# Kernel tuning notes

Hardware: AMD Instinct MI355X
Metric: run time of the kernel (lower is better)

The kernel has to match this reference:

```python
import jax, jax.numpy as jnp
import numpy as np

NUM_SEQ, NUM_RES = 512, 768
MSA_C, PAIR_C, NUM_HEAD = 64, 128, 8
VALUE_DIM = MSA_C // NUM_HEAD
EPS = 1e-5


def _layernorm(x, scale, bias):
    mu = jnp.mean(x, axis=-1, keepdims=True)
    var = jnp.var(x, axis=-1, keepdims=True)
    return (x - mu) * jax.lax.rsqrt(var + EPS) * scale + bias


def setup_inputs() -> dict:
    key = jax.random.key(0)
    ks = jax.random.split(key, 8)
    act = jax.random.normal(ks[0], (NUM_SEQ, NUM_RES, MSA_C), dtype=jnp.float32)
    mask = jnp.ones((NUM_SEQ, NUM_RES), dtype=jnp.float32)
    pair_act = jax.random.normal(ks[1], (NUM_RES, NUM_RES, PAIR_C), dtype=jnp.float32)
    # learned params
    act_scale = jnp.ones((MSA_C,), jnp.float32)
    act_bias = jnp.zeros((MSA_C,), jnp.float32)
    pair_scale = jnp.ones((PAIR_C,), jnp.float32)
    pair_bias = jnp.zeros((PAIR_C,), jnp.float32)
    w_pair_logits = jax.random.normal(ks[2], (NUM_HEAD, PAIR_C), jnp.float32) * (PAIR_C ** -0.5)
    v_proj = jax.random.normal(ks[3], (MSA_C, NUM_HEAD, VALUE_DIM), jnp.float32) * (MSA_C ** -0.5)
    w_gate = jax.random.normal(ks[4], (MSA_C, MSA_C), jnp.float32) * (MSA_C ** -0.5)
    w_out = jax.random.normal(ks[5], (MSA_C, MSA_C), jnp.float32) * (MSA_C ** -0.5)
    return {
        "act": act, "mask": mask, "pair_act": pair_act,
        "act_scale": act_scale, "act_bias": act_bias,
        "pair_scale": pair_scale, "pair_bias": pair_bias,
        "w_pair_logits": w_pair_logits, "v_proj": v_proj,
        "w_gate": w_gate, "w_out": w_out,
    }


def reference(act, mask, pair_act, act_scale, act_bias, pair_scale, pair_bias,
              w_pair_logits, v_proj, w_gate, w_out):
    act = _layernorm(act, act_scale, act_bias)            # [b, k, i]
    pair = _layernorm(pair_act, pair_scale, pair_bias)    # [q, k, c]
    logits = jnp.einsum('qkc,hc->hqk', pair, w_pair_logits)  # [h, q, k]
    # mask reduced over MSA rows; torch casts to bf16 before the bias add
    mask_max = jnp.max(mask, axis=0).astype(jnp.bfloat16)    # [k]
    logits = logits + 1e9 * (mask_max.astype(logits.dtype) - 1.0)
    weights = jax.nn.softmax(logits, axis=-1)                # [h, q, k]
    v = jnp.einsum('bki,ihc->bkhc', act, v_proj)             # [b, k, h, c]
    v_avg = jnp.einsum('hqk,bkhc->bqhc', weights, v)         # [b, q, h, c]
    v_avg = v_avg.reshape(v_avg.shape[0], v_avg.shape[1], -1)  # [b, q, h*c]
    gate = jax.nn.sigmoid(act @ w_gate.T)
    return (v_avg * gate) @ w_out.T
```

## Files before the change

kernel.cpp:

```cpp
#include <hip/hip_runtime.h>
#include <hip/hip_bf16.h>

#define NSEQ 512
#define NRES 768
#define MSAC 64
#define PAIRC 128
#define NHEAD 8

typedef __attribute__((ext_vector_type(8))) short short8_t;
typedef __attribute__((ext_vector_type(4))) float f32x4;

__device__ __forceinline__ float bf2f(unsigned short u){
  return __uint_as_float(((unsigned int)u) << 16);
}
__device__ __forceinline__ unsigned short f2bf(float f){
  unsigned int x = __float_as_uint(f);
  x += 0x7fffu + ((x >> 16) & 1u);
  return (unsigned short)(x >> 16);
}
__device__ __forceinline__ void glds16(const void* g, void* l){
  __builtin_amdgcn_global_load_lds(
      (const __attribute__((address_space(1))) unsigned int*)g,
      (__attribute__((address_space(3))) unsigned int*)l, 16, 0, 0);
}

__global__ __launch_bounds__(256) void k_prep2(
    const float* __restrict__ mask, const float* __restrict__ vproj,
    const float* __restrict__ wgate, const float* __restrict__ wout,
    float* __restrict__ bias, unsigned short* __restrict__ WvT,
    unsigned short* __restrict__ WgT, unsigned short* __restrict__ WoH,
    unsigned short* __restrict__ WoL)
{
  const int bid = blockIdx.x, tid = threadIdx.x;
  if (bid < 12){
    __shared__ float red[4][64];
    const int kk = bid*64 + (tid & 63);
    const int bs = tid >> 6;
    float m = -1e30f;
    for (int b = bs; b < NSEQ; b += 4) m = fmaxf(m, mask[(size_t)b*NRES + kk]);
    red[bs][tid & 63] = m;
    __syncthreads();
    if (tid < 64){
      float mm = fmaxf(fmaxf(red[0][tid], red[1][tid]),
                       fmaxf(red[2][tid], red[3][tid]));
      bias[bid*64 + tid] = 1e9f * (bf2f(f2bf(mm)) - 1.0f);
    }
  } else {
    const int t = (bid - 12)*256 + tid;
    const int j = t >> 6, i = t & 63;
    WvT[t] = f2bf(vproj[i*64 + j]);
    WgT[t] = f2bf(wgate[t]);
    float wv = wout[t];
    unsigned short hh = f2bf(wv);
    WoH[t] = hh;
    WoL[t] = f2bf(wv - bf2f(hh));
  }
}

__global__ __launch_bounds__(256) void k_pairact(
    const float* __restrict__ pair, const float* __restrict__ pscale,
    const float* __restrict__ pbias, const float* __restrict__ wl,
    const float* __restrict__ mbias, unsigned short* __restrict__ weights,
    const float* __restrict__ act, const float* __restrict__ ascale,
    const float* __restrict__ abias, const unsigned short* __restrict__ WvT,
    const unsigned short* __restrict__ WgT, unsigned short* __restrict__ v,
    unsigned short* __restrict__ gate)
{
  __shared__ __align__(16) unsigned char sm[24576];
  const int bid = blockIdx.x;
  const int tid = threadIdx.x;

  if (bid < 768){
    float (*lg)[NRES] = (float (*)[NRES])sm;
    const int q = bid;
    const int wv = tid >> 6, lane = tid & 63;
    const int g = lane & 7;
    const int c0 = g * 16;

    float scl[16], bsl[16];
    #pragma unroll
    for (int i = 0; i < 4; ++i){
      float4 s4 = *(const float4*)(pscale + c0 + i*4);
      float4 b4 = *(const float4*)(pbias  + c0 + i*4);
      scl[4*i+0]=s4.x; scl[4*i+1]=s4.y; scl[4*i+2]=s4.z; scl[4*i+3]=s4.w;
      bsl[4*i+0]=b4.x; bsl[4*i+1]=b4.y; bsl[4*i+2]=b4.z; bsl[4*i+3]=b4.w;
    }
    unsigned int wp[8][8];
    #pragma unroll
    for (int h = 0; h < 8; ++h){
      #pragma unroll
      for (int jj = 0; jj < 8; ++jj){
        float2 w2 = *(const float2*)(wl + h*PAIRC + c0 + jj*2);
        wp[h][jj] = (unsigned int)f2bf(w2.x) | ((unsigned int)f2bf(w2.y) << 16);
      }
    }

    for (int it = 0; it < 24; ++it){
      int k = it*32 + wv*8 + (lane >> 3);
      const float* prow = pair + ((size_t)q * NRES + k) * PAIRC + c0;
      float x[16];
      #pragma unroll
      for (int i = 0; i < 4; ++i){
        float4 v4 = *(const float4*)(prow + i*4);
        x[4*i+0]=v4.x; x[4*i+1]=v4.y; x[4*i+2]=v4.z; x[4*i+3]=v4.w;
      }
      float s = 0.f, ss = 0.f;
      #pragma unroll
      for (int i = 0; i < 16; ++i){ s += x[i]; ss += x[i]*x[i]; }
      #pragma unroll
      for (int m = 1; m < 8; m <<= 1){
        s  += __shfl_xor(s,  m, 64);
        ss += __shfl_xor(ss, m, 64);
      }
      float mu  = s * (1.f/128.f);
      float var = ss * (1.f/128.f) - mu*mu;
      float rs  = rsqrtf(var + 1e-5f);
      #pragma unroll
      for (int i = 0; i < 16; ++i) x[i] = (x[i] - mu) * rs * scl[i] + bsl[i];
      float ph[8];
      #pragma unroll
      for (int h = 0; h < 8; ++h){
        float p = 0.f;
        #pragma unroll
        for (int jj = 0; jj < 8; ++jj){
          unsigned int w = wp[h][jj];
          float wlo = __uint_as_float(w << 16);
          float whi = __uint_as_float(w & 0xffff0000u);
          p += x[2*jj] * wlo + x[2*jj+1] * whi;
        }
        ph[h] = p;
      }
      #pragma unroll
      for (int h = 0; h < 8; ++h){
        #pragma unroll
        for (int m = 1; m < 8; m <<= 1) ph[h] += __shfl_xor(ph[h], m, 64);
      }
      #pragma unroll
      for (int h = 0; h < 8; ++h) if (g == h) lg[h][k] = ph[h];
    }
    __syncthreads();
    #pragma unroll
    for (int hh = 0; hh < 2; ++hh){
      int h = wv + hh*4;
      float mx = -1e30f;
      for (int kk = lane; kk < NRES; kk += 64) mx = fmaxf(mx, lg[h][kk] + mbias[kk]);
      #pragma unroll
      for (int m = 1; m < 64; m <<= 1) mx = fmaxf(mx, __shfl_xor(mx, m, 64));
      float sum = 0.f;
      for (int kk = lane; kk < NRES; kk += 64){
        float e = __expf(lg[h][kk] + mbias[kk] - mx);
        lg[h][kk] = e; sum += e;
      }
      #pragma unroll
      for (int m = 1; m < 64; m <<= 1) sum += __shfl_xor(sum, m, 64);
      float inv = 1.0f / sum;
      unsigned short* wrow = weights + ((size_t)h * NRES + q) * NRES;
      for (int kk = lane; kk < NRES; kk += 64) wrow[kk] = f2bf(lg[h][kk] * inv);
    }
  } else {
    unsigned short (*vt)[72] = (unsigned short (*)[72])sm;
    unsigned short (*gt)[72] = (unsigned short (*)[72])(sm + 9216);
    const int abid = bid - 768;
    const int b  = abid / 12;
    const int k0 = (abid % 12) * 64;
    const int w = tid >> 6, lane = tid & 63;
    const int lr = lane & 15;
    const int lc = lane >> 4;
    const int row = k0 + w*16 + lr;

    const float* arow = act + ((size_t)b*NRES + row)*MSAC;
    float x[2][8];
    #pragma unroll
    for (int s = 0; s < 2; ++s){
      float4 t0 = *(const float4*)(arow + s*32 + lc*8);
      float4 t1 = *(const float4*)(arow + s*32 + lc*8 + 4);
      x[s][0]=t0.x; x[s][1]=t0.y; x[s][2]=t0.z; x[s][3]=t0.w;
      x[s][4]=t1.x; x[s][5]=t1.y; x[s][6]=t1.z; x[s][7]=t1.w;
    }
    float ps = 0.f, pss = 0.f;
    #pragma unroll
    for (int s = 0; s < 2; ++s)
      #pragma unroll
      for (int e = 0; e < 8; ++e){ ps += x[s][e]; pss += x[s][e]*x[s][e]; }
    ps  += __shfl_xor(ps, 16, 64);  pss += __shfl_xor(pss, 16, 64);
    ps  += __shfl_xor(ps, 32, 64);  pss += __shfl_xor(pss, 32, 64);
    const float mu  = ps * (1.f/64.f);
    const float var = pss * (1.f/64.f) - mu*mu;
    const float rs  = rsqrtf(var + 1e-5f);

    short8_t a[2];
    #pragma unroll
    for (int s = 0; s < 2; ++s){
      float4 s0 = *(const float4*)(ascale + s*32 + lc*8);
      float4 s1 = *(const float4*)(ascale + s*32 + lc*8 + 4);
      float4 b0 = *(const float4*)(abias  + s*32 + lc*8);
      float4 b1 = *(const float4*)(abias  + s*32 + lc*8 + 4);
      const float sc[8] = {s0.x,s0.y,s0.z,s0.w,s1.x,s1.y,s1.z,s1.w};
      const float bs[8] = {b0.x,b0.y,b0.z,b0.w,b1.x,b1.y,b1.z,b1.w};
      #pragma unroll
      for (int e = 0; e < 8; ++e)
        a[s][e] = (short)f2bf((x[s][e] - mu)*rs*sc[e] + bs[e]);
    }

    short8_t bv[4][2], bg[4][2];
    #pragma unroll
    for (int mf = 0; mf < 4; ++mf){
      #pragma unroll
      for (int s = 0; s < 2; ++s){
        bv[mf][s] = *(const short8_t*)(WvT + (mf*16 + lr)*64 + s*32 + lc*8);
        bg[mf][s] = *(const short8_t*)(WgT + (mf*16 + lr)*64 + s*32 + lc*8);
      }
    }

    f32x4 accv[4], accg[4];
    #pragma unroll
    for (int mf = 0; mf < 4; ++mf){ accv[mf] = 0.f; accg[mf] = 0.f; }
    #pragma unroll
    for (int mf = 0; mf < 4; ++mf){
      #pragma unroll
      for (int s = 0; s < 2; ++s){
        accv[mf] = __builtin_amdgcn_mfma_f32_16x16x32_bf16(a[s], bv[mf][s], accv[mf], 0, 0, 0);
        accg[mf] = __builtin_amdgcn_mfma_f32_16x16x32_bf16(bg[mf][s], a[s], accg[mf], 0, 0, 0);
      }
    }

    #pragma unroll
    for (int mf = 0; mf < 4; ++mf){
      ushort4 ov;
      ov.x = f2bf(accv[mf][0]); ov.y = f2bf(accv[mf][1]);
      ov.z = f2bf(accv[mf][2]); ov.w = f2bf(accv[mf][3]);
      *(ushort4*)&vt[mf*16 + lr][w*16 + lc*4] = ov;
      ushort4 og;
      og.x = f2bf(1.0f/(1.0f + __expf(-accg[mf][0])));
      og.y = f2bf(1.0f/(1.0f + __expf(-accg[mf][1])));
      og.z = f2bf(1.0f/(1.0f + __expf(-accg[mf][2])));
      og.w = f2bf(1.0f/(1.0f + __expf(-accg[mf][3])));
      *(ushort4*)&gt[w*16 + lr][mf*16 + lc*4] = og;
    }
    __syncthreads();
    #pragma unroll
    for (int it = 0; it < 2; ++it){
      int fl = it*256 + tid;
      int j = fl >> 3, chunk = fl & 7;
      uint4 val = *(const uint4*)&vt[j][chunk*8];
      *(uint4*)(v + ((size_t)(j >> 3)*4096 + (size_t)b*8 + (j & 7))*NRES + k0 + chunk*8) = val;
    }
    #pragma unroll
    for (int it = 0; it < 2; ++it){
      int fl = it*256 + tid;
      int k = fl >> 3, chunk = fl & 7;
      uint4 val = *(const uint4*)&gt[k][chunk*8];
      *(uint4*)(gate + ((size_t)b*NRES + k0 + k)*MSAC + chunk*8) = val;
    }
  }
}

__global__ __launch_bounds__(256) void k_wavg(
    const unsigned short* __restrict__ V, const unsigned short* __restrict__ W,
    unsigned short* __restrict__ Y)
{
  __shared__ unsigned char smem[32768];

  const int flat = blockIdx.x;
  const int nid  = (flat & 7) * 192 + (flat >> 3);
  const int m    = nid % 192;
  const int by   = m % 6;
  const int bx   = m / 6;
  const int h    = nid / 192;

  const int tid = threadIdx.x, wid = tid >> 6, lane = tid & 63;
  const int wm = wid & 1, wn = wid >> 1;
  const unsigned short* Ag = V + (size_t)h*4096*768 + (size_t)bx*128*768;
  const unsigned short* Bg = W + (size_t)h*768*768 + (size_t)by*128*768;

  f32x4 acc[4][4];
  #pragma unroll
  for (int i=0;i<4;++i){
    #pragma unroll
    for (int jj=0;jj<4;++jj) acc[i][jj] = 0.f;
  }

  #define STAGE_K(bufsel, kt) { \
    unsigned char* Ab = smem + (bufsel)*16384; \
    unsigned char* Bb = Ab + 8192; \
    _Pragma("unroll") \
    for (int r = 0; r < 2; ++r){ \
      int cid = tid + r*256; \
      int rw = cid >> 2, ch = cid & 3; \
      int sc = ch ^ ((rw >> 1) & 3); \
      glds16(Ag + (size_t)rw*768 + (kt)*32 + sc*8, Ab + cid*16 - lane*16); \
      glds16(Bg + (size_t)rw*768 + (kt)*32 + sc*8, Bb + cid*16 - lane*16); \
    } }

  STAGE_K(0, 0);
  __syncthreads();
  const int c0 = lane >> 4;
  for (int kt = 0; kt < 24; ++kt){
    if (kt < 23) STAGE_K((kt+1)&1, kt+1);
    unsigned char* Ab = smem + (kt&1)*16384;
    unsigned char* Bb = Ab + 8192;
    short8_t af[4], bf[4];
    #pragma unroll
    for (int mf = 0; mf < 4; ++mf){
      int row = wm*64 + mf*16 + (lane & 15);
      int off = row*64 + ((c0 ^ ((row>>1)&3)) << 4);
      af[mf] = *(const short8_t*)(Ab + off);
    }
    #pragma unroll
    for (int nf = 0; nf < 4; ++nf){
      int row = wn*64 + nf*16 + (lane & 15);
      int off = row*64 + ((c0 ^ ((row>>1)&3)) << 4);
      bf[nf] = *(const short8_t*)(Bb + off);
    }
    #pragma unroll
    for (int mf = 0; mf < 4; ++mf){
      #pragma unroll
      for (int nf = 0; nf < 4; ++nf)
        acc[mf][nf] = __builtin_amdgcn_mfma_f32_16x16x32_bf16(af[mf], bf[nf], acc[mf][nf], 0, 0, 0);
    }
    __syncthreads();
  }
  #undef STAGE_K

  unsigned char* Ds = smem;
  #pragma unroll
  for (int mf = 0; mf < 4; ++mf){
    int bc = wm*64 + mf*16 + ((lane >> 4) << 2);
    #pragma unroll
    for (int nf = 0; nf < 4; ++nf){
      int q = wn*64 + nf*16 + (lane & 15);
      f32x4 a = acc[mf][nf];
      ushort4 o;
      o.x = f2bf(a[0]); o.y = f2bf(a[1]); o.z = f2bf(a[2]); o.w = f2bf(a[3]);
      int off = q*256 + bc*2; off ^= (q & 7) << 4;
      *(ushort4*)(Ds + off) = o;
    }
  }
  __syncthreads();
  unsigned short* Yb = Y + ((size_t)(h*32 + bx)*768 + by*128)*128;
  #pragma unroll
  for (int it = 0; it < 8; ++it){
    int fl = it*256 + tid;
    int q = fl >> 4, chunk = fl & 15;
    int off = q*256 + chunk*16; off ^= (q & 7) << 4;
    uint4 val = *(const uint4*)(Ds + off);
    *(uint4*)(Yb + (size_t)fl*8) = val;
  }
}

__global__ __launch_bounds__(256) void k_final(
    const unsigned short* __restrict__ Y, const unsigned short* __restrict__ gate,
    const unsigned short* __restrict__ WoH, const unsigned short* __restrict__ WoL,
    float* __restrict__ out)
{
  const int p = blockIdx.x;
  const int r = p & 7, t = p >> 3;
  const int b  = r*64 + (t & 63);
  const int q0 = (t >> 6) * 64;
  const int tid = threadIdx.x, w = tid >> 6, lane = tid & 63;
  const int lr = lane & 15, lc = lane >> 4;

  short8_t bh[4][2], bl[4][2];
  #pragma unroll
  for (int nf = 0; nf < 4; ++nf){
    #pragma unroll
    for (int s = 0; s < 2; ++s){
      bh[nf][s] = *(const short8_t*)(WoH + (nf*16 + lr)*64 + s*32 + lc*8);
      bl[nf][s] = *(const short8_t*)(WoL + (nf*16 + lr)*64 + s*32 + lc*8);
    }
  }

  const int q = q0 + w*16 + lr;
  short8_t ah[2], al[2];
  #pragma unroll
  for (int s = 0; s < 2; ++s){
    const int hh = s*4 + lc;
    short8_t y8 = *(const short8_t*)(Y + ((size_t)(hh*32 + (b >> 4))*768 + q)*128 + (b & 15)*8);
    short8_t g8 = *(const short8_t*)(gate + ((size_t)b*NRES + q)*MSAC + s*32 + lc*8);
    #pragma unroll
    for (int e = 0; e < 8; ++e){
      float pp = bf2f((unsigned short)y8[e]) * bf2f((unsigned short)g8[e]);
      unsigned short hi = f2bf(pp);
      ah[s][e] = (short)hi;
      al[s][e] = (short)f2bf(pp - bf2f(hi));
    }
  }

  f32x4 acc[4];
  #pragma unroll
  for (int nf = 0; nf < 4; ++nf) acc[nf] = 0.f;
  #pragma unroll
  for (int nf = 0; nf < 4; ++nf){
    #pragma unroll
    for (int s = 0; s < 2; ++s){
      acc[nf] = __builtin_amdgcn_mfma_f32_16x16x32_bf16(ah[s], bh[nf][s], acc[nf], 0, 0, 0);
      acc[nf] = __builtin_amdgcn_mfma_f32_16x16x32_bf16(al[s], bh[nf][s], acc[nf], 0, 0, 0);
      acc[nf] = __builtin_amdgcn_mfma_f32_16x16x32_bf16(ah[s], bl[nf][s], acc[nf], 0, 0, 0);
    }
  }

  #pragma unroll
  for (int nf = 0; nf < 4; ++nf){
    #pragma unroll
    for (int e = 0; e < 4; ++e){
      int qq = q0 + w*16 + lc*4 + e;
      out[((size_t)b*NRES + qq)*MSAC + nf*16 + lr] = acc[nf][e];
    }
  }
}

extern "C" void kernel_launch(void* const* d_in, const int* in_sizes, int n_in,
                              void* d_out, int out_size, void* d_ws, size_t ws_size,
                              hipStream_t stream) {
  (void)in_sizes; (void)n_in; (void)out_size; (void)ws_size;
  const float* act    = (const float*)d_in[0];
  const float* mask   = (const float*)d_in[1];
  const float* pair   = (const float*)d_in[2];
  const float* ascale = (const float*)d_in[3];
  const float* abias  = (const float*)d_in[4];
  const float* pscale = (const float*)d_in[5];
  const float* pbias  = (const float*)d_in[6];
  const float* wl     = (const float*)d_in[7];
  const float* vproj  = (const float*)d_in[8];
  const float* wgate  = (const float*)d_in[9];
  const float* wout   = (const float*)d_in[10];
  float* out = (float*)d_out;

  char* ws = (char*)d_ws;
  float*          mbias   = (float*)(ws);
  unsigned short* WvT     = (unsigned short*)(ws + 4096);
  unsigned short* WgT     = (unsigned short*)(ws + 12288);
  unsigned short* WoH     = (unsigned short*)(ws + 20480);
  unsigned short* WoL     = (unsigned short*)(ws + 28672);
  unsigned short* weights = (unsigned short*)(ws + 36864);
  unsigned short* v       = (unsigned short*)(ws + 36864 + 9437184);
  unsigned short* gate    = (unsigned short*)(ws + 36864 + 9437184 + 50331648);
  unsigned short* y       = (unsigned short*)(ws + 36864 + 9437184 + 2*50331648ull);

  k_prep2<<<dim3(28), dim3(256), 0, stream>>>(mask, vproj, wgate, wout,
                                              mbias, WvT, WgT, WoH, WoL);
  k_pairact<<<dim3(6912), dim3(256), 0, stream>>>(pair, pscale, pbias, wl, mbias, weights,
                                                  act, ascale, abias, WvT, WgT, v, gate);
  k_wavg<<<dim3(1536), dim3(256), 0, stream>>>(v, weights, y);
  k_final<<<dim3(6144), dim3(256), 0, stream>>>(y, gate, WoH, WoL, out);
}
```

Measured before the change: 331.3 us.

## Compute pair logits with MFMA after folding layernorm scale into weights

The pair-logit projection in k_pairact moves from per-lane scalar FMAs with shuffle reductions to bf16 MFMA 16x16x32. Because the layernorm is linear, it is rewritten as rsq*(W'·x - mu*A) + B, where W' = scale*w is precomputed in k_prep2 as hi/lo bf16 pairs and A, B are precomputed per head. The raw inputs are split into hi and lo bf16 parts to keep accuracy close to fp32. This removes most of the VALU work in the logits stage, but it adds conversion work, a second MFMA per step, and a mean-subtraction step that can lose precision.

```diff
diff --git a/kernel.cpp b/kernel.cpp
--- a/kernel.cpp
+++ b/kernel.cpp
@@ -27,9 +27,12 @@
 __global__ __launch_bounds__(256) void k_prep2(
     const float* __restrict__ mask, const float* __restrict__ vproj,
     const float* __restrict__ wgate, const float* __restrict__ wout,
+    const float* __restrict__ pscale, const float* __restrict__ pbias,
+    const float* __restrict__ wl,
     float* __restrict__ bias, unsigned short* __restrict__ WvT,
     unsigned short* __restrict__ WgT, unsigned short* __restrict__ WoH,
-    unsigned short* __restrict__ WoL)
+    unsigned short* __restrict__ WoL, unsigned short* __restrict__ WST,
+    float* __restrict__ AB)
 {
   const int bid = blockIdx.x, tid = threadIdx.x;
   if (bid < 12){
@@ -45,7 +48,7 @@
                        fmaxf(red[2][tid], red[3][tid]));
       bias[bid*64 + tid] = 1e9f * (bf2f(f2bf(mm)) - 1.0f);
     }
-  } else {
+  } else if (bid < 28){
     const int t = (bid - 12)*256 + tid;
     const int j = t >> 6, i = t & 63;
     WvT[t] = f2bf(vproj[i*64 + j]);
@@ -54,13 +57,35 @@
     unsigned short hh = f2bf(wv);
     WoH[t] = hh;
     WoL[t] = f2bf(wv - bf2f(hh));
+  } else {
+    #pragma unroll
+    for (int i = 0; i < 4; ++i){
+      int t = i*256 + tid;
+      int h = t >> 7, c = t & 127;
+      float w = pscale[c] * wl[h*PAIRC + c];
+      unsigned short hh = f2bf(w);
+      WST[h*PAIRC + c] = hh;
+      WST[(h + 8)*PAIRC + c] = f2bf(w - bf2f(hh));
+    }
+    const int h = tid >> 5, cc = tid & 31;
+    float pa = 0.f, pb = 0.f;
+    for (int c = cc; c < PAIRC; c += 32){
+      float w = wl[h*PAIRC + c];
+      pa += pscale[c]*w;  pb += pbias[c]*w;
+    }
+    #pragma unroll
+    for (int m = 1; m < 32; m <<= 1){
+      pa += __shfl_xor(pa, m, 64);
+      pb += __shfl_xor(pb, m, 64);
+    }
+    if (cc == 0){ AB[h] = pa; AB[8 + h] = pb; }
   }
 }
 
 __global__ __launch_bounds__(256) void k_pairact(
-    const float* __restrict__ pair, const float* __restrict__ pscale,
-    const float* __restrict__ pbias, const float* __restrict__ wl,
-    const float* __restrict__ mbias, unsigned short* __restrict__ weights,
+    const float* __restrict__ pair, const unsigned short* __restrict__ WST,
+    const float* __restrict__ AB, const float* __restrict__ mbias,
+    unsigned short* __restrict__ weights,
     const float* __restrict__ act, const float* __restrict__ ascale,
     const float* __restrict__ abias, const unsigned short* __restrict__ WvT,
     const unsigned short* __restrict__ WgT, unsigned short* __restrict__ v,
@@ -74,69 +99,54 @@
     float (*lg)[NRES] = (float (*)[NRES])sm;
     const int q = bid;
     const int wv = tid >> 6, lane = tid & 63;
-    const int g = lane & 7;
-    const int c0 = g * 16;
-
-    float scl[16], bsl[16];
-    #pragma unroll
-    for (int i = 0; i < 4; ++i){
-      float4 s4 = *(const float4*)(pscale + c0 + i*4);
-      float4 b4 = *(const float4*)(pbias  + c0 + i*4);
-      scl[4*i+0]=s4.x; scl[4*i+1]=s4.y; scl[4*i+2]=s4.z; scl[4*i+3]=s4.w;
-      bsl[4*i+0]=b4.x; bsl[4*i+1]=b4.y; bsl[4*i+2]=b4.z; bsl[4*i+3]=b4.w;
-    }
-    unsigned int wp[8][8];
-    #pragma unroll
-    for (int h = 0; h < 8; ++h){
-      #pragma unroll
-      for (int jj = 0; jj < 8; ++jj){
-        float2 w2 = *(const float2*)(wl + h*PAIRC + c0 + jj*2);
-        wp[h][jj] = (unsigned int)f2bf(w2.x) | ((unsigned int)f2bf(w2.y) << 16);
+    const int lr = lane & 15, lcq = lane >> 4;
+
+    short8_t wfrag[4];
+    #pragma unroll
+    for (int s = 0; s < 4; ++s)
+      wfrag[s] = *(const short8_t*)(WST + lr*PAIRC + lcq*8 + s*32);
+
+    const int hb = (lcq & 1) * 4;
+    float A4[4], B4[4];
+    #pragma unroll
+    for (int r = 0; r < 4; ++r){ A4[r] = AB[hb + r]; B4[r] = AB[8 + hb + r]; }
+
+    for (int tile = wv; tile < 48; tile += 4){
+      const int k0 = tile * 16;
+      const float* base = pair + ((size_t)q*NRES + k0 + lr)*PAIRC + lcq*8;
+      f32x4 a1 = 0.f, a2 = 0.f;
+      float s = 0.f, ss = 0.f;
+      #pragma unroll
+      for (int st = 0; st < 4; ++st){
+        float4 u0 = *(const float4*)(base + st*32);
+        float4 u1 = *(const float4*)(base + st*32 + 4);
+        float xv[8] = {u0.x,u0.y,u0.z,u0.w,u1.x,u1.y,u1.z,u1.w};
+        short8_t xh, xl;
+        #pragma unroll
+        for (int e = 0; e < 8; ++e){
+          s += xv[e]; ss += xv[e]*xv[e];
+          unsigned short hi = f2bf(xv[e]);
+          xh[e] = (short)hi;
+          xl[e] = (short)f2bf(xv[e] - bf2f(hi));
+        }
+        a1 = __builtin_amdgcn_mfma_f32_16x16x32_bf16(wfrag[st], xh, a1, 0, 0, 0);
+        a2 = __builtin_amdgcn_mfma_f32_16x16x32_bf16(wfrag[st], xl, a2, 0, 0, 0);
       }
-    }
-
-    for (int it = 0; it < 24; ++it){
-      int k = it*32 + wv*8 + (lane >> 3);
-      const float* prow = pair + ((size_t)q * NRES + k) * PAIRC + c0;
-      float x[16];
-      #pragma unroll
-      for (int i = 0; i < 4; ++i){
-        float4 v4 = *(const float4*)(prow + i*4);
-        x[4*i+0]=v4.x; x[4*i+1]=v4.y; x[4*i+2]=v4.z; x[4*i+3]=v4.w;
+      s  += __shfl_xor(s, 16, 64);  ss += __shfl_xor(ss, 16, 64);
+      s  += __shfl_xor(s, 32, 64);  ss += __shfl_xor(ss, 32, 64);
+      const float mu  = s * (1.f/128.f);
+      const float var = ss * (1.f/128.f) - mu*mu;
+      const float rsq = rsqrtf(var + 1e-5f);
+      float d[4];
+      #pragma unroll
+      for (int r = 0; r < 4; ++r)
+        d[r] = a1[r] + __shfl_xor(a1[r], 32, 64) + a2[r];
+      if (lane < 32){
+        const int k = k0 + lr;
+        #pragma unroll
+        for (int r = 0; r < 4; ++r)
+          lg[hb + r][k] = rsq * (d[r] - mu * A4[r]) + B4[r];
       }
-      float s = 0.f, ss = 0.f;
-      #pragma unroll
-      for (int i = 0; i < 16; ++i){ s += x[i]; ss += x[i]*x[i]; }
-      #pragma unroll
-      for (int m = 1; m < 8; m <<= 1){
-        s  += __shfl_xor(s,  m, 64);
-        ss += __shfl_xor(ss, m, 64);
-      }
-      float mu  = s * (1.f/128.f);
-      float var = ss * (1.f/128.f) - mu*mu;
-      float rs  = rsqrtf(var + 1e-5f);
-      #pragma unroll
-      for (int i = 0; i < 16; ++i) x[i] = (x[i] - mu) * rs * scl[i] + bsl[i];
-      float ph[8];
-      #pragma unroll
-      for (int h = 0; h < 8; ++h){
-        float p = 0.f;
-        #pragma unroll
-        for (int jj = 0; jj < 8; ++jj){
-          unsigned int w = wp[h][jj];
-          float wlo = __uint_as_float(w << 16);
-          float whi = __uint_as_float(w & 0xffff0000u);
-          p += x[2*jj] * wlo + x[2*jj+1] * whi;
-        }
-        ph[h] = p;
-      }
-      #pragma unroll
-      for (int h = 0; h < 8; ++h){
-        #pragma unroll
-        for (int m = 1; m < 8; m <<= 1) ph[h] += __shfl_xor(ph[h], m, 64);
-      }
-      #pragma unroll
-      for (int h = 0; h < 8; ++h) if (g == h) lg[h][k] = ph[h];
     }
     __syncthreads();
     #pragma unroll
@@ -432,14 +442,17 @@
   unsigned short* WgT     = (unsigned short*)(ws + 12288);
   unsigned short* WoH     = (unsigned short*)(ws + 20480);
   unsigned short* WoL     = (unsigned short*)(ws + 28672);
-  unsigned short* weights = (unsigned short*)(ws + 36864);
-  unsigned short* v       = (unsigned short*)(ws + 36864 + 9437184);
-  unsigned short* gate    = (unsigned short*)(ws + 36864 + 9437184 + 50331648);
-  unsigned short* y       = (unsigned short*)(ws + 36864 + 9437184 + 2*50331648ull);
-
-  k_prep2<<<dim3(28), dim3(256), 0, stream>>>(mask, vproj, wgate, wout,
-                                              mbias, WvT, WgT, WoH, WoL);
-  k_pairact<<<dim3(6912), dim3(256), 0, stream>>>(pair, pscale, pbias, wl, mbias, weights,
+  unsigned short* WST     = (unsigned short*)(ws + 36864);
+  float*          AB      = (float*)(ws + 40960);
+  unsigned short* weights = (unsigned short*)(ws + 45056);
+  unsigned short* v       = (unsigned short*)(ws + 45056 + 9437184);
+  unsigned short* gate    = (unsigned short*)(ws + 45056 + 9437184 + 50331648);
+  unsigned short* y       = (unsigned short*)(ws + 45056 + 9437184 + 2*50331648ull);
+
+  k_prep2<<<dim3(29), dim3(256), 0, stream>>>(mask, vproj, wgate, wout,
+                                              pscale, pbias, wl,
+                                              mbias, WvT, WgT, WoH, WoL, WST, AB);
+  k_pairact<<<dim3(6912), dim3(256), 0, stream>>>(pair, WST, AB, mbias, weights,
                                                   act, ascale, abias, WvT, WgT, v, gate);
   k_wavg<<<dim3(1536), dim3(256), 0, stream>>>(v, weights, y);
   k_final<<<dim3(6144), dim3(256), 0, stream>>>(y, gate, WoH, WoL, out);
```

Result: faster. 307.7 us (-7.1%).
